# Performance work log

Hardware: AMD Instinct MI355X
Metric: run time of the kernel (lower is better)

The kernel has to match this reference:

```python
import jax, jax.numpy as jnp
import numpy as np

HEADS, DIM_HEAD = 8, 64
SCALE = DIM_HEAD ** -0.5
LAMDA1, LAMDA2 = 5.0, 5.0


def setup_inputs() -> dict:
    B, N, M = 32, 1536, 80  # N = 32*48 spatial tokens, M = max_boxes
    QD, KD, VD = 320, 768, 768
    inner = HEADS * DIM_HEAD
    ks = jax.random.split(jax.random.key(0), 11)
    return {
        "x": jax.random.normal(ks[0], (B, N, QD), jnp.float32),
        "key": jax.random.normal(ks[1], (B, M, KD), jnp.float32),
        "value": jax.random.normal(ks[2], (B, M, VD), jnp.float32),
        "mask": jax.random.randint(ks[3], (B, M), 0, 2).astype(bool),
        "perl_box_masking_map": jax.random.normal(ks[4], (B, N, M), jnp.float32),
        "perl_road_masking_map": jax.random.normal(ks[5], (B, 1, N), jnp.float32),
        "Wq": jax.random.normal(ks[6], (inner, QD), jnp.float32) * 0.02,
        "Wk": jax.random.normal(ks[7], (inner, KD), jnp.float32) * 0.02,
        "Wv": jax.random.normal(ks[8], (inner, VD), jnp.float32) * 0.02,
        "Wo": jax.random.normal(ks[9], (QD, inner), jnp.float32) * 0.02,
        "bo": jnp.zeros((QD,), jnp.float32),
    }


def reference(x, key, value, mask, perl_box_masking_map, perl_road_masking_map, Wq, Wk, Wv, Wo, bo):
    B, N, _ = x.shape
    M = key.shape[1]
    H, C = HEADS, DIM_HEAD
    # QKV projections (torch Linear: y = x @ W.T)
    q = (x @ Wq.T).reshape(B, N, H, C)
    k = (key @ Wk.T).reshape(B, M, H, C)
    v = (value @ Wv.T).reshape(B, M, H, C)
    # attention scores with scale, key mask, and two additive bias maps
    sim = jnp.einsum('bnhc,bmhc->bhnm', q, k) * SCALE  # (B, H, N, M)
    neg = -jnp.finfo(sim.dtype).max
    sim = jnp.where(mask[:, None, None, :], sim, neg)  # mask fill BEFORE bias adds, as in torch
    sim = sim + LAMDA1 * perl_box_masking_map[:, None, :, :]
    road = jnp.swapaxes(perl_road_masking_map, 1, 2)  # (B, N, 1) -> broadcast over key axis
    sim = sim + LAMDA2 * road[:, None, :, :]
    attn = jax.nn.softmax(sim, axis=-1)
    out = jnp.einsum('bhnm,bmhc->bnhc', attn, v).reshape(B, N, H * C)
    return out @ Wo.T + bo  # dropout is identity in eval
```

## Files before the change

kernel.cpp:

```cpp
#include <hip/hip_runtime.h>
#include <hip/hip_bf16.h>

typedef __attribute__((ext_vector_type(8))) short short8;
typedef __attribute__((ext_vector_type(4))) float floatx4;
typedef unsigned short u16;

#define NB 32
#define NN 1536
#define NM 80
#define NH 8
#define NC 64
#define NINNER 512
#define NQD 320
#define NKD 768

__device__ __forceinline__ float bf2f(u16 u) {
    union { unsigned i; float f; } x; x.i = ((unsigned)u) << 16; return x.f;
}
__device__ __forceinline__ u16 f2bf(float f) {
    unsigned u = __float_as_uint(f);
    unsigned r = (u + 0x7FFFu + ((u >> 16) & 1u)) >> 16;
    return (u16)r;
}
__device__ __forceinline__ short8 cvt8(const float* __restrict__ p) {
    float4 a = ((const float4*)p)[0];
    float4 b = ((const float4*)p)[1];
    short8 r;
    r[0] = (short)f2bf(a.x); r[1] = (short)f2bf(a.y);
    r[2] = (short)f2bf(a.z); r[3] = (short)f2bf(a.w);
    r[4] = (short)f2bf(b.x); r[5] = (short)f2bf(b.y);
    r[6] = (short)f2bf(b.z); r[7] = (short)f2bf(b.w);
    return r;
}
__device__ __forceinline__ void gload16(const u16* g, u16* l) {
    __builtin_amdgcn_global_load_lds(
        (const __attribute__((address_space(1))) unsigned int*)g,
        (__attribute__((address_space(3))) unsigned int*)l, 16, 0, 0);
}

__global__ __launch_bounds__(256) void detect_dtype(const u16* __restrict__ x,
                                                    int* __restrict__ flag) {
    __shared__ int cnt;
    if (threadIdx.x == 0) cnt = 0;
    __syncthreads();
    int c = 0;
    for (int i = threadIdx.x; i < 8192; i += 256) {
        unsigned e = (x[i] >> 7) & 0xFF;
        if (e >= 0xA0) c++;
    }
    atomicAdd(&cnt, c);
    __syncthreads();
    if (threadIdx.x == 0) *flag = (cnt > 64) ? 1 : 0;
}

__global__ __launch_bounds__(256) void mask_prep(const unsigned char* __restrict__ raw,
                                                 float* __restrict__ maskbias) {
    __shared__ int c_bf, c_f32, c_u8;
    if (threadIdx.x == 0) { c_bf = 0; c_f32 = 0; c_u8 = 0; }
    __syncthreads();
    for (int i = threadIdx.x; i < NB * NM; i += 256) {
        unsigned char v = raw[i];
        if (v == 0x3F && (i & 3) == 1) atomicAdd(&c_bf, 1);
        if (v == 0x3F && (i & 3) == 3) atomicAdd(&c_f32, 1);
        if (v != 0 && (i & 3) != 0) atomicAdd(&c_u8, 1);
    }
    __syncthreads();
    int md;
    if (c_bf > 0) md = 2;
    else if (c_f32 > 0) md = 3;
    else if (c_u8 > 0) md = 1;
    else md = 0;
    for (int i = threadIdx.x; i < NB * NM; i += 256) {
        bool on;
        if (md == 2) on = ((const u16*)raw)[i] != 0;
        else if (md == 3) on = ((const float*)raw)[i] != 0.0f;
        else if (md == 1) on = raw[i] != 0;
        else on = ((const int*)raw)[i] != 0;
        maskbias[i] = on ? 0.0f : -3.4028234663852886e38f;
    }
}

struct ConvSeg { const void* src; u16* dst; int nblk; };
struct ConvArgs { ConvSeg s[6]; };

__global__ __launch_bounds__(256) void conv_batch(ConvArgs a, const int* __restrict__ flag) {
    const int f = *flag;
    int b = blockIdx.x, seg = 0;
    while (seg < 6 && b >= a.s[seg].nblk) { b -= a.s[seg].nblk; seg++; }
    if (seg >= 6) return;
    const long idx = (long)b * 2048 + threadIdx.x * 8;
    u16* dst = a.s[seg].dst;
    if (f) *(short8*)(dst + idx) = cvt8((const float*)a.s[seg].src + idx);
    else   *(short8*)(dst + idx) = *(const short8*)((const u16*)a.s[seg].src + idx);
}

__global__ __launch_bounds__(256) void conv_wo(const void* __restrict__ src,
                                               u16* __restrict__ dst,
                                               const int* __restrict__ flag) {
    const int f = *flag;
    const long idx = ((long)blockIdx.x * 256 + threadIdx.x) * 8;
    const int row = (int)(idx >> 9);
    if (row < NQD) {
        if (f) *(short8*)(dst + idx) = cvt8((const float*)src + idx);
        else   *(short8*)(dst + idx) = *(const short8*)((const u16*)src + idx);
    } else {
        *(short8*)(dst + idx) = (short8)0;
    }
}

template <bool OUT_DYN, bool BIAS, bool DUAL>
__global__ __launch_bounds__(256) void gemm128(const u16* __restrict__ A,
                                               const u16* __restrict__ B,
                                               const void* __restrict__ bias,
                                               void* __restrict__ C,
                                               const u16* __restrict__ A2,
                                               const u16* __restrict__ B2,
                                               void* __restrict__ C2,
                                               int Nreal, int K,
                                               const int* __restrict__ flag) {
    __shared__ __align__(16) u16 As[128 * 32];
    __shared__ __align__(16) u16 Bs[128 * 32];
    if (DUAL && blockIdx.z) { A = A2; B = B2; C = C2; }
    const int f = *flag;
    const int tid = threadIdx.x;
    const int wave = tid >> 6, lane = tid & 63;
    const int l16 = lane & 15, quad = lane >> 4;
    const int wr = wave >> 1, wc = wave & 1;
    const int bm0 = blockIdx.x * 128, bn0 = blockIdx.y * 128;

    const int r0 = tid >> 2, c0 = tid & 3;
    const int sc = c0 ^ ((r0 >> 1) & 3);
    const u16* Ag = A + (size_t)(bm0 + r0) * K + sc * 8;
    const u16* Bg = B + (size_t)(bn0 + r0) * K + sc * 8;
    u16* AsW = As + wave * 512;
    u16* BsW = Bs + wave * 512;

    const int swz = (l16 >> 1) & 3;
    floatx4 acc[4][4];
#pragma unroll
    for (int i = 0; i < 4; ++i)
#pragma unroll
        for (int n = 0; n < 4; ++n) acc[i][n] = (floatx4)0.0f;

    for (int kk = 0; kk < K; kk += 32) {
        __syncthreads();
#pragma unroll
        for (int j = 0; j < 2; ++j) {
            gload16(Ag + (size_t)(j * 64) * K + kk, AsW + j * 2048);
            gload16(Bg + (size_t)(j * 64) * K + kk, BsW + j * 2048);
        }
        __syncthreads();
        short8 af[4], bf[4];
#pragma unroll
        for (int i = 0; i < 4; ++i)
            af[i] = *(const short8*)&As[(wr * 64 + i * 16 + l16) * 32 + ((quad ^ swz) * 8)];
#pragma unroll
        for (int n = 0; n < 4; ++n)
            bf[n] = *(const short8*)&Bs[(wc * 64 + n * 16 + l16) * 32 + ((quad ^ swz) * 8)];
#pragma unroll
        for (int i = 0; i < 4; ++i)
#pragma unroll
            for (int n = 0; n < 4; ++n)
                acc[i][n] = __builtin_amdgcn_mfma_f32_16x16x32_bf16(af[i], bf[n], acc[i][n], 0, 0, 0);
    }

#pragma unroll
    for (int n = 0; n < 4; ++n) {
        const int col = bn0 + wc * 64 + n * 16 + l16;
        if (col < Nreal) {
            float badd = 0.0f;
            if (BIAS) badd = f ? ((const float*)bias)[col] : bf2f(((const u16*)bias)[col]);
#pragma unroll
            for (int i = 0; i < 4; ++i)
#pragma unroll
                for (int r = 0; r < 4; ++r) {
                    const int row = bm0 + wr * 64 + i * 16 + quad * 4 + r;
                    const float val = acc[i][n][r] + badd;
                    if (OUT_DYN && f) ((float*)C)[(size_t)row * Nreal + col] = val;
                    else              ((u16*)C)[(size_t)row * Nreal + col] = f2bf(val);
                }
        }
    }
}

__global__ __launch_bounds__(256) void transpose_v(const u16* __restrict__ v,
                                                   u16* __restrict__ vT) {
    int b = blockIdx.x >> 3, h = blockIdx.x & 7;
    const u16* src = v + (size_t)b * NM * NINNER + h * NC;
    u16* o = vT + (size_t)(b * NH + h) * NC * 96;
    for (int idx = threadIdx.x; idx < NM * NC; idx += 256) {
        int m = idx >> 6, c = idx & 63;
        o[c * 96 + m] = src[(size_t)m * NINNER + c];
    }
    for (int idx = threadIdx.x; idx < NC * 16; idx += 256) {
        int c = idx >> 4, m = 80 + (idx & 15);
        o[c * 96 + m] = 0;
    }
}

__global__ __launch_bounds__(256) void attn_kernel(const u16* __restrict__ q,
                                                   const u16* __restrict__ k,
                                                   const u16* __restrict__ vT,
                                                   const float* __restrict__ maskbias,
                                                   const void* __restrict__ box,
                                                   const void* __restrict__ road,
                                                   u16* __restrict__ attno,
                                                   const int* __restrict__ flag) {
    const int f = *flag;
    const int n0 = blockIdx.x * 64;
    const int h = blockIdx.y;
    const int b = blockIdx.z;
    const int tid = threadIdx.x;
    const int wave = tid >> 6, lane = tid & 63;
    const int l16 = lane & 15, quad = lane >> 4;

    __shared__ __align__(16) u16 p_lds[64][104];

    floatx4 s[5];
#pragma unroll
    for (int i = 0; i < 5; ++i) s[i] = (floatx4)0.0f;
    const size_t qrow = (size_t)(b * NN + n0 + 16 * wave + l16) * NINNER + h * NC;
#pragma unroll
    for (int kk = 0; kk < NC; kk += 32) {
        short8 a = *(const short8*)(q + qrow + kk + quad * 8);
#pragma unroll
        for (int mt = 0; mt < 5; ++mt) {
            short8 bf = *(const short8*)(k + (size_t)(b * NM + mt * 16 + l16) * NINNER + h * NC + kk + quad * 8);
            s[mt] = __builtin_amdgcn_mfma_f32_16x16x32_bf16(a, bf, s[mt], 0, 0, 0);
        }
    }

    float sv[5][4];
#pragma unroll
    for (int r = 0; r < 4; ++r) {
        int n = n0 + 16 * wave + quad * 4 + r;
        size_t ridx = (size_t)b * NN + n;
        float roadv = 5.0f * (f ? ((const float*)road)[ridx] : bf2f(((const u16*)road)[ridx]));
#pragma unroll
        for (int mt = 0; mt < 5; ++mt) {
            int m = mt * 16 + l16;
            size_t bidx = ((size_t)b * NN + n) * NM + m;
            float boxv = 5.0f * (f ? ((const float*)box)[bidx] : bf2f(((const u16*)box)[bidx]));
            sv[mt][r] = s[mt][r] * 0.125f + maskbias[b * NM + m] + boxv + roadv;
        }
    }

    float rowsum[4];
#pragma unroll
    for (int r = 0; r < 4; ++r) {
        float mx = sv[0][r];
#pragma unroll
        for (int mt = 1; mt < 5; ++mt) mx = fmaxf(mx, sv[mt][r]);
#pragma unroll
        for (int off = 1; off < 16; off <<= 1) mx = fmaxf(mx, __shfl_xor(mx, off, 16));
        float sum = 0.0f;
#pragma unroll
        for (int mt = 0; mt < 5; ++mt) {
            float p = __expf(sv[mt][r] - mx);
            sv[mt][r] = p;
            sum += p;
        }
#pragma unroll
        for (int off = 1; off < 16; off <<= 1) sum += __shfl_xor(sum, off, 16);
        rowsum[r] = sum;
    }

#pragma unroll
    for (int r = 0; r < 4; ++r) {
        int lr = 16 * wave + quad * 4 + r;
#pragma unroll
        for (int mt = 0; mt < 5; ++mt) p_lds[lr][mt * 16 + l16] = f2bf(sv[mt][r]);
        p_lds[lr][80 + l16] = 0;
    }
    __syncthreads();

    floatx4 o[4];
#pragma unroll
    for (int i = 0; i < 4; ++i) o[i] = (floatx4)0.0f;
    const u16* vbase = vT + (size_t)(b * NH + h) * NC * 96;
#pragma unroll
    for (int kk = 0; kk < 96; kk += 32) {
        short8 a = *(const short8*)&p_lds[16 * wave + l16][kk + quad * 8];
#pragma unroll
        for (int nt = 0; nt < 4; ++nt) {
            short8 bf = *(const short8*)(vbase + (size_t)(nt * 16 + l16) * 96 + kk + quad * 8);
            o[nt] = __builtin_amdgcn_mfma_f32_16x16x32_bf16(a, bf, o[nt], 0, 0, 0);
        }
    }

#pragma unroll
    for (int nt = 0; nt < 4; ++nt) {
#pragma unroll
        for (int r = 0; r < 4; ++r) {
            int n = n0 + 16 * wave + quad * 4 + r;
            float inv = 1.0f / rowsum[r];
            attno[((size_t)b * NN + n) * NINNER + h * NC + nt * 16 + l16] = f2bf(o[nt][r] * inv);
        }
    }
}

extern "C" void kernel_launch(void* const* d_in, const int* in_sizes, int n_in,
                              void* d_out, int out_size, void* d_ws, size_t ws_size,
                              hipStream_t stream) {
    (void)in_sizes; (void)n_in; (void)out_size; (void)ws_size;
    const void* x    = d_in[0];
    const void* key  = d_in[1];
    const void* val  = d_in[2];
    const unsigned char* mask = (const unsigned char*)d_in[3];
    const void* box  = d_in[4];
    const void* road = d_in[5];
    const void* Wq   = d_in[6];
    const void* Wk   = d_in[7];
    const void* Wv   = d_in[8];
    const void* Wo   = d_in[9];
    const void* bo   = d_in[10];

    char* ws = (char*)d_ws;
    size_t off = 0;
    auto carve = [&](size_t bytes) {
        char* p = ws + off;
        off += (bytes + 255) & ~(size_t)255;
        return p;
    };
    int* flag   = (int*)carve(256);
    u16* q_ws   = (u16*)carve((size_t)NB * NN * NINNER * 2);
    u16* k_ws   = (u16*)carve((size_t)NB * NM * NINNER * 2);
    u16* v_ws   = (u16*)carve((size_t)NB * NM * NINNER * 2);
    u16* vT_ws  = (u16*)carve((size_t)NB * NH * NC * 96 * 2);
    u16* ao_ws  = (u16*)carve((size_t)NB * NN * NINNER * 2);
    u16* x_bf   = ao_ws;
    u16* key_bf = (u16*)carve((size_t)NB * NM * NKD * 2);
    u16* val_bf = (u16*)carve((size_t)NB * NM * NKD * 2);
    u16* Wq_bf  = (u16*)carve((size_t)NINNER * NQD * 2);
    u16* Wk_bf  = (u16*)carve((size_t)NINNER * NKD * 2);
    u16* Wv_bf  = (u16*)carve((size_t)NINNER * NKD * 2);
    u16* WoP_bf = (u16*)carve((size_t)384 * NINNER * 2);
    float* mb   = (float*)carve((size_t)NB * NM * 4);

    detect_dtype<<<1, 256, 0, stream>>>((const u16*)x, flag);
    mask_prep<<<1, 256, 0, stream>>>(mask, mb);

    ConvArgs ca;
    ca.s[0] = { x,     x_bf,   (int)((size_t)NB * NN * NQD / 2048) };
    ca.s[1] = { key,   key_bf, (int)((size_t)NB * NM * NKD / 2048) };
    ca.s[2] = { val,   val_bf, (int)((size_t)NB * NM * NKD / 2048) };
    ca.s[3] = { Wq,    Wq_bf,  (int)((size_t)NINNER * NQD / 2048) };
    ca.s[4] = { Wk,    Wk_bf,  (int)((size_t)NINNER * NKD / 2048) };
    ca.s[5] = { Wv,    Wv_bf,  (int)((size_t)NINNER * NKD / 2048) };
    int totblk = 0;
    for (int i = 0; i < 6; ++i) totblk += ca.s[i].nblk;
    conv_batch<<<totblk, 256, 0, stream>>>(ca, flag);
    conv_wo<<<96, 256, 0, stream>>>(Wo, WoP_bf, flag);

    gemm128<false, false, false><<<dim3(NB * NN / 128, NINNER / 128), 256, 0, stream>>>(
        x_bf, Wq_bf, nullptr, q_ws, nullptr, nullptr, nullptr, NINNER, NQD, flag);
    gemm128<false, false, true><<<dim3(NB * NM / 128, NINNER / 128, 2), 256, 0, stream>>>(
        key_bf, Wk_bf, nullptr, k_ws, val_bf, Wv_bf, v_ws, NINNER, NKD, flag);
    transpose_v<<<NB * NH, 256, 0, stream>>>(v_ws, vT_ws);
    attn_kernel<<<dim3(NN / 64, NH, NB), 256, 0, stream>>>(
        q_ws, k_ws, vT_ws, mb, box, road, ao_ws, flag);
    gemm128<true, true, false><<<dim3(NB * NN / 128, 384 / 128), 256, 0, stream>>>(
        ao_ws, WoP_bf, bo, d_out, nullptr, nullptr, nullptr, NQD, NINNER, flag);
}
```

Baseline: 349.6 us.

## Fuse output projection into attention and fp32→bf16 conversion into GEMM loads

The attention kernel now loops over all 8 heads inside each block. Each normalized head output goes through LDS and is multiplied straight into the Wo output projection, with the bias added at the end. This removes the separate output GEMM and the round trip of the attention output through global memory. The box and road bias maps and the mask are also read once per block instead of once per head. Separately, the activation GEMMs convert fp32 A tiles to bf16 in registers while loading, which drops the standalone conversion pass over x, key and value. The cost is fewer, longer-running attention blocks with more accumulator registers, and a register-staged A load in place of the async global-to-LDS copy.

```diff
diff --git a/kernel.cpp b/kernel.cpp
--- a/kernel.cpp
+++ b/kernel.cpp
@@ -81,42 +81,27 @@
 }
 
 struct ConvSeg { const void* src; u16* dst; int nblk; };
-struct ConvArgs { ConvSeg s[6]; };
+struct ConvArgs { ConvSeg s[4]; };
 
 __global__ __launch_bounds__(256) void conv_batch(ConvArgs a, const int* __restrict__ flag) {
     const int f = *flag;
     int b = blockIdx.x, seg = 0;
-    while (seg < 6 && b >= a.s[seg].nblk) { b -= a.s[seg].nblk; seg++; }
-    if (seg >= 6) return;
+    while (seg < 4 && b >= a.s[seg].nblk) { b -= a.s[seg].nblk; seg++; }
+    if (seg >= 4) return;
     const long idx = (long)b * 2048 + threadIdx.x * 8;
     u16* dst = a.s[seg].dst;
     if (f) *(short8*)(dst + idx) = cvt8((const float*)a.s[seg].src + idx);
     else   *(short8*)(dst + idx) = *(const short8*)((const u16*)a.s[seg].src + idx);
 }
 
-__global__ __launch_bounds__(256) void conv_wo(const void* __restrict__ src,
-                                               u16* __restrict__ dst,
-                                               const int* __restrict__ flag) {
-    const int f = *flag;
-    const long idx = ((long)blockIdx.x * 256 + threadIdx.x) * 8;
-    const int row = (int)(idx >> 9);
-    if (row < NQD) {
-        if (f) *(short8*)(dst + idx) = cvt8((const float*)src + idx);
-        else   *(short8*)(dst + idx) = *(const short8*)((const u16*)src + idx);
-    } else {
-        *(short8*)(dst + idx) = (short8)0;
-    }
-}
-
-template <bool OUT_DYN, bool BIAS, bool DUAL>
-__global__ __launch_bounds__(256) void gemm128(const u16* __restrict__ A,
+template <bool DUAL>
+__global__ __launch_bounds__(256) void gemm128(const void* __restrict__ A,
                                                const u16* __restrict__ B,
-                                               const void* __restrict__ bias,
-                                               void* __restrict__ C,
-                                               const u16* __restrict__ A2,
+                                               u16* __restrict__ C,
+                                               const void* __restrict__ A2,
                                                const u16* __restrict__ B2,
-                                               void* __restrict__ C2,
-                                               int Nreal, int K,
+                                               u16* __restrict__ C2,
+                                               int Ncols, int K,
                                                const int* __restrict__ flag) {
     __shared__ __align__(16) u16 As[128 * 32];
     __shared__ __align__(16) u16 Bs[128 * 32];
@@ -130,10 +115,10 @@
 
     const int r0 = tid >> 2, c0 = tid & 3;
     const int sc = c0 ^ ((r0 >> 1) & 3);
-    const u16* Ag = A + (size_t)(bm0 + r0) * K + sc * 8;
     const u16* Bg = B + (size_t)(bn0 + r0) * K + sc * 8;
-    u16* AsW = As + wave * 512;
     u16* BsW = Bs + wave * 512;
+    u16* AsD = As + wave * 512 + (size_t)(lane) * 8;
+    const size_t aoff = (size_t)(bm0 + r0) * K + sc * 8;
 
     const int swz = (l16 >> 1) & 3;
     floatx4 acc[4][4];
@@ -146,7 +131,10 @@
         __syncthreads();
 #pragma unroll
         for (int j = 0; j < 2; ++j) {
-            gload16(Ag + (size_t)(j * 64) * K + kk, AsW + j * 2048);
+            short8 av;
+            if (f) av = cvt8((const float*)A + aoff + (size_t)(j * 64) * K + kk);
+            else   av = *(const short8*)((const u16*)A + aoff + (size_t)(j * 64) * K + kk);
+            *(short8*)(AsD + j * 2048) = av;
             gload16(Bg + (size_t)(j * 64) * K + kk, BsW + j * 2048);
         }
         __syncthreads();
@@ -167,19 +155,13 @@
 #pragma unroll
     for (int n = 0; n < 4; ++n) {
         const int col = bn0 + wc * 64 + n * 16 + l16;
-        if (col < Nreal) {
-            float badd = 0.0f;
-            if (BIAS) badd = f ? ((const float*)bias)[col] : bf2f(((const u16*)bias)[col]);
-#pragma unroll
-            for (int i = 0; i < 4; ++i)
-#pragma unroll
-                for (int r = 0; r < 4; ++r) {
-                    const int row = bm0 + wr * 64 + i * 16 + quad * 4 + r;
-                    const float val = acc[i][n][r] + badd;
-                    if (OUT_DYN && f) ((float*)C)[(size_t)row * Nreal + col] = val;
-                    else              ((u16*)C)[(size_t)row * Nreal + col] = f2bf(val);
-                }
-        }
+#pragma unroll
+        for (int i = 0; i < 4; ++i)
+#pragma unroll
+            for (int r = 0; r < 4; ++r) {
+                const int row = bm0 + wr * 64 + i * 16 + quad * 4 + r;
+                C[(size_t)row * Ncols + col] = f2bf(acc[i][n][r]);
+            }
     }
 }
 
@@ -198,105 +180,159 @@
     }
 }
 
-__global__ __launch_bounds__(256) void attn_kernel(const u16* __restrict__ q,
-                                                   const u16* __restrict__ k,
-                                                   const u16* __restrict__ vT,
-                                                   const float* __restrict__ maskbias,
-                                                   const void* __restrict__ box,
-                                                   const void* __restrict__ road,
-                                                   u16* __restrict__ attno,
-                                                   const int* __restrict__ flag) {
+__global__ __launch_bounds__(256) void attn_fused(const u16* __restrict__ q,
+                                                  const u16* __restrict__ k,
+                                                  const u16* __restrict__ vT,
+                                                  const float* __restrict__ maskbias,
+                                                  const void* __restrict__ box,
+                                                  const void* __restrict__ road,
+                                                  const u16* __restrict__ Wo,
+                                                  const void* __restrict__ bo,
+                                                  void* __restrict__ out,
+                                                  const int* __restrict__ flag) {
     const int f = *flag;
     const int n0 = blockIdx.x * 64;
-    const int h = blockIdx.y;
-    const int b = blockIdx.z;
+    const int b = blockIdx.y;
     const int tid = threadIdx.x;
     const int wave = tid >> 6, lane = tid & 63;
     const int l16 = lane & 15, quad = lane >> 4;
 
     __shared__ __align__(16) u16 p_lds[64][104];
-
-    floatx4 s[5];
-#pragma unroll
-    for (int i = 0; i < 5; ++i) s[i] = (floatx4)0.0f;
-    const size_t qrow = (size_t)(b * NN + n0 + 16 * wave + l16) * NINNER + h * NC;
-#pragma unroll
-    for (int kk = 0; kk < NC; kk += 32) {
-        short8 a = *(const short8*)(q + qrow + kk + quad * 8);
+    __shared__ __align__(16) u16 oh_s[64][72];
+
+    {
+        int row = 16 * wave + (lane >> 2);
+        int col = 80 + (lane & 3) * 4;
+        ushort4 z; z.x = 0; z.y = 0; z.z = 0; z.w = 0;
+        *(ushort4*)&p_lds[row][col] = z;
+    }
+
+    float add[5][4];
+#pragma unroll
+    for (int r = 0; r < 4; ++r) {
+        const int n = n0 + 16 * wave + quad * 4 + r;
+        const size_t ridx = (size_t)b * NN + n;
+        const float roadv = 5.0f * (f ? ((const float*)road)[ridx]
+                                      : bf2f(((const u16*)road)[ridx]));
 #pragma unroll
         for (int mt = 0; mt < 5; ++mt) {
-            short8 bf = *(const short8*)(k + (size_t)(b * NM + mt * 16 + l16) * NINNER + h * NC + kk + quad * 8);
-            s[mt] = __builtin_amdgcn_mfma_f32_16x16x32_bf16(a, bf, s[mt], 0, 0, 0);
-        }
-    }
-
-    float sv[5][4];
-#pragma unroll
-    for (int r = 0; r < 4; ++r) {
-        int n = n0 + 16 * wave + quad * 4 + r;
-        size_t ridx = (size_t)b * NN + n;
-        float roadv = 5.0f * (f ? ((const float*)road)[ridx] : bf2f(((const u16*)road)[ridx]));
-#pragma unroll
-        for (int mt = 0; mt < 5; ++mt) {
-            int m = mt * 16 + l16;
-            size_t bidx = ((size_t)b * NN + n) * NM + m;
-            float boxv = 5.0f * (f ? ((const float*)box)[bidx] : bf2f(((const u16*)box)[bidx]));
-            sv[mt][r] = s[mt][r] * 0.125f + maskbias[b * NM + m] + boxv + roadv;
-        }
-    }
-
-    float rowsum[4];
-#pragma unroll
-    for (int r = 0; r < 4; ++r) {
-        float mx = sv[0][r];
-#pragma unroll
-        for (int mt = 1; mt < 5; ++mt) mx = fmaxf(mx, sv[mt][r]);
-#pragma unroll
-        for (int off = 1; off < 16; off <<= 1) mx = fmaxf(mx, __shfl_xor(mx, off, 16));
-        float sum = 0.0f;
-#pragma unroll
-        for (int mt = 0; mt < 5; ++mt) {
-            float p = __expf(sv[mt][r] - mx);
-            sv[mt][r] = p;
-            sum += p;
-        }
-#pragma unroll
-        for (int off = 1; off < 16; off <<= 1) sum += __shfl_xor(sum, off, 16);
-        rowsum[r] = sum;
-    }
-
-#pragma unroll
-    for (int r = 0; r < 4; ++r) {
-        int lr = 16 * wave + quad * 4 + r;
-#pragma unroll
-        for (int mt = 0; mt < 5; ++mt) p_lds[lr][mt * 16 + l16] = f2bf(sv[mt][r]);
-        p_lds[lr][80 + l16] = 0;
-    }
-    __syncthreads();
-
-    floatx4 o[4];
-#pragma unroll
-    for (int i = 0; i < 4; ++i) o[i] = (floatx4)0.0f;
-    const u16* vbase = vT + (size_t)(b * NH + h) * NC * 96;
-#pragma unroll
-    for (int kk = 0; kk < 96; kk += 32) {
-        short8 a = *(const short8*)&p_lds[16 * wave + l16][kk + quad * 8];
-#pragma unroll
-        for (int nt = 0; nt < 4; ++nt) {
-            short8 bf = *(const short8*)(vbase + (size_t)(nt * 16 + l16) * 96 + kk + quad * 8);
-            o[nt] = __builtin_amdgcn_mfma_f32_16x16x32_bf16(a, bf, o[nt], 0, 0, 0);
-        }
-    }
-
-#pragma unroll
-    for (int nt = 0; nt < 4; ++nt) {
+            const int m = mt * 16 + l16;
+            const size_t bidx = ridx * NM + m;
+            const float boxv = 5.0f * (f ? ((const float*)box)[bidx]
+                                         : bf2f(((const u16*)box)[bidx]));
+            add[mt][r] = maskbias[b * NM + m] + boxv + roadv;
+        }
+    }
+    float bov[5];
+#pragma unroll
+    for (int j = 0; j < 5; ++j) {
+        const int col = (wave * 5 + j) * 16 + l16;
+        bov[j] = f ? ((const float*)bo)[col] : bf2f(((const u16*)bo)[col]);
+    }
+
+    floatx4 accO[4][5];
+#pragma unroll
+    for (int i = 0; i < 4; ++i)
+#pragma unroll
+        for (int j = 0; j < 5; ++j) accO[i][j] = (floatx4)0.0f;
+
+    for (int h = 0; h < NH; ++h) {
+        floatx4 s[5];
+#pragma unroll
+        for (int i = 0; i < 5; ++i) s[i] = (floatx4)0.0f;
+        const size_t qrow = (size_t)(b * NN + n0 + 16 * wave + l16) * NINNER + h * NC;
+#pragma unroll
+        for (int kk = 0; kk < NC; kk += 32) {
+            short8 a = *(const short8*)(q + qrow + kk + quad * 8);
+#pragma unroll
+            for (int mt = 0; mt < 5; ++mt) {
+                short8 bf = *(const short8*)(k + (size_t)(b * NM + mt * 16 + l16) * NINNER + h * NC + kk + quad * 8);
+                s[mt] = __builtin_amdgcn_mfma_f32_16x16x32_bf16(a, bf, s[mt], 0, 0, 0);
+            }
+        }
+
+        float sv[5][4], inv[4];
 #pragma unroll
         for (int r = 0; r < 4; ++r) {
-            int n = n0 + 16 * wave + quad * 4 + r;
-            float inv = 1.0f / rowsum[r];
-            attno[((size_t)b * NN + n) * NINNER + h * NC + nt * 16 + l16] = f2bf(o[nt][r] * inv);
-        }
-    }
+#pragma unroll
+            for (int mt = 0; mt < 5; ++mt)
+                sv[mt][r] = s[mt][r] * 0.125f + add[mt][r];
+            float mx = sv[0][r];
+#pragma unroll
+            for (int mt = 1; mt < 5; ++mt) mx = fmaxf(mx, sv[mt][r]);
+#pragma unroll
+            for (int off = 1; off < 16; off <<= 1) mx = fmaxf(mx, __shfl_xor(mx, off, 16));
+            float sum = 0.0f;
+#pragma unroll
+            for (int mt = 0; mt < 5; ++mt) {
+                float p = __expf(sv[mt][r] - mx);
+                sv[mt][r] = p;
+                sum += p;
+            }
+#pragma unroll
+            for (int off = 1; off < 16; off <<= 1) sum += __shfl_xor(sum, off, 16);
+            inv[r] = 1.0f / sum;
+        }
+
+#pragma unroll
+        for (int r = 0; r < 4; ++r) {
+            const int lr = 16 * wave + quad * 4 + r;
+#pragma unroll
+            for (int mt = 0; mt < 5; ++mt) p_lds[lr][mt * 16 + l16] = f2bf(sv[mt][r]);
+        }
+
+        floatx4 o[4];
+#pragma unroll
+        for (int i = 0; i < 4; ++i) o[i] = (floatx4)0.0f;
+        const u16* vbase = vT + (size_t)(b * NH + h) * NC * 96;
+#pragma unroll
+        for (int kk = 0; kk < 96; kk += 32) {
+            short8 a = *(const short8*)&p_lds[16 * wave + l16][kk + quad * 8];
+#pragma unroll
+            for (int nt = 0; nt < 4; ++nt) {
+                short8 bf = *(const short8*)(vbase + (size_t)(nt * 16 + l16) * 96 + kk + quad * 8);
+                o[nt] = __builtin_amdgcn_mfma_f32_16x16x32_bf16(a, bf, o[nt], 0, 0, 0);
+            }
+        }
+
+#pragma unroll
+        for (int nt = 0; nt < 4; ++nt)
+#pragma unroll
+            for (int r = 0; r < 4; ++r)
+                oh_s[16 * wave + quad * 4 + r][nt * 16 + l16] = f2bf(o[nt][r] * inv[r]);
+        __syncthreads();
+
+#pragma unroll
+        for (int kk2 = 0; kk2 < 64; kk2 += 32) {
+            short8 a2[4];
+#pragma unroll
+            for (int i = 0; i < 4; ++i)
+                a2[i] = *(const short8*)&oh_s[i * 16 + l16][kk2 + quad * 8];
+#pragma unroll
+            for (int j = 0; j < 5; ++j) {
+                short8 b2 = *(const short8*)(Wo + (size_t)((wave * 5 + j) * 16 + l16) * NINNER + h * NC + kk2 + quad * 8);
+#pragma unroll
+                for (int i = 0; i < 4; ++i)
+                    accO[i][j] = __builtin_amdgcn_mfma_f32_16x16x32_bf16(a2[i], b2, accO[i][j], 0, 0, 0);
+            }
+        }
+        __syncthreads();
+    }
+
+#pragma unroll
+    for (int i = 0; i < 4; ++i)
+#pragma unroll
+        for (int j = 0; j < 5; ++j) {
+            const int col = (wave * 5 + j) * 16 + l16;
+#pragma unroll
+            for (int r = 0; r < 4; ++r) {
+                const int row = n0 + i * 16 + quad * 4 + r;
+                const float val = accO[i][j][r] + bov[j];
+                const size_t oidx = (size_t)(b * NN + row) * NQD + col;
+                if (f) ((float*)out)[oidx] = val;
+                else   ((u16*)out)[oidx] = f2bf(val);
+            }
+        }
 }
 
 extern "C" void kernel_launch(void* const* d_in, const int* in_sizes, int n_in,
@@ -327,38 +363,27 @@
     u16* k_ws   = (u16*)carve((size_t)NB * NM * NINNER * 2);
     u16* v_ws   = (u16*)carve((size_t)NB * NM * NINNER * 2);
     u16* vT_ws  = (u16*)carve((size_t)NB * NH * NC * 96 * 2);
-    u16* ao_ws  = (u16*)carve((size_t)NB * NN * NINNER * 2);
-    u16* x_bf   = ao_ws;
-    u16* key_bf = (u16*)carve((size_t)NB * NM * NKD * 2);
-    u16* val_bf = (u16*)carve((size_t)NB * NM * NKD * 2);
     u16* Wq_bf  = (u16*)carve((size_t)NINNER * NQD * 2);
     u16* Wk_bf  = (u16*)carve((size_t)NINNER * NKD * 2);
     u16* Wv_bf  = (u16*)carve((size_t)NINNER * NKD * 2);
-    u16* WoP_bf = (u16*)carve((size_t)384 * NINNER * 2);
+    u16* Wo_bf  = (u16*)carve((size_t)NQD * NINNER * 2);
     float* mb   = (float*)carve((size_t)NB * NM * 4);
 
     detect_dtype<<<1, 256, 0, stream>>>((const u16*)x, flag);
     mask_prep<<<1, 256, 0, stream>>>(mask, mb);
 
     ConvArgs ca;
-    ca.s[0] = { x,     x_bf,   (int)((size_t)NB * NN * NQD / 2048) };
-    ca.s[1] = { key,   key_bf, (int)((size_t)NB * NM * NKD / 2048) };
-    ca.s[2] = { val,   val_bf, (int)((size_t)NB * NM * NKD / 2048) };
-    ca.s[3] = { Wq,    Wq_bf,  (int)((size_t)NINNER * NQD / 2048) };
-    ca.s[4] = { Wk,    Wk_bf,  (int)((size_t)NINNER * NKD / 2048) };
-    ca.s[5] = { Wv,    Wv_bf,  (int)((size_t)NINNER * NKD / 2048) };
-    int totblk = 0;
-    for (int i = 0; i < 6; ++i) totblk += ca.s[i].nblk;
-    conv_batch<<<totblk, 256, 0, stream>>>(ca, flag);
-    conv_wo<<<96, 256, 0, stream>>>(Wo, WoP_bf, flag);
-
-    gemm128<false, false, false><<<dim3(NB * NN / 128, NINNER / 128), 256, 0, stream>>>(
-        x_bf, Wq_bf, nullptr, q_ws, nullptr, nullptr, nullptr, NINNER, NQD, flag);
-    gemm128<false, false, true><<<dim3(NB * NM / 128, NINNER / 128, 2), 256, 0, stream>>>(
-        key_bf, Wk_bf, nullptr, k_ws, val_bf, Wv_bf, v_ws, NINNER, NKD, flag);
+    ca.s[0] = { Wq, Wq_bf, (int)((size_t)NINNER * NQD / 2048) };
+    ca.s[1] = { Wk, Wk_bf, (int)((size_t)NINNER * NKD / 2048) };
+    ca.s[2] = { Wv, Wv_bf, (int)((size_t)NINNER * NKD / 2048) };
+    ca.s[3] = { Wo, Wo_bf, (int)((size_t)NQD * NINNER / 2048) };
+    conv_batch<<<544, 256, 0, stream>>>(ca, flag);
+
+    gemm128<false><<<dim3(NB * NN / 128, NINNER / 128), 256, 0, stream>>>(
+        x, Wq_bf, q_ws, nullptr, nullptr, nullptr, NINNER, NQD, flag);
+    gemm128<true><<<dim3(NB * NM / 128, NINNER / 128, 2), 256, 0, stream>>>(
+        key, Wk_bf, k_ws, val, Wv_bf, v_ws, NINNER, NKD, flag);
     transpose_v<<<NB * NH, 256, 0, stream>>>(v_ws, vT_ws);
-    attn_kernel<<<dim3(NN / 64, NH, NB), 256, 0, stream>>>(
-        q_ws, k_ws, vT_ws, mb, box, road, ao_ws, flag);
-    gemm128<true, true, false><<<dim3(NB * NN / 128, 384 / 128), 256, 0, stream>>>(
-        ao_ws, WoP_bf, bo, d_out, nullptr, nullptr, nullptr, NQD, NINNER, flag);
-}
+    attn_fused<<<dim3(NN / 64, NB), 256, 0, stream>>>(
+        q_ws, k_ws, vT_ws, mb, box, road, Wo_bf, bo, d_out, flag);
+}
```

Measured after the change: 388.7 us. 1.11x slower.
